# Optimization experiments

Measured on AMD Instinct MI355X. Metric: run time of the kernel, lower is better.

Reference implementation:

```python
import jax, jax.numpy as jnp
import numpy as np

D = 4
R = 6
P = 2 * R + 1          # 13, fine match window
N = P * P              # 169
MR = 12
MP = 2 * MR + 1        # 25, coarse search window
DIL_INT = 15


def corr_sampler(t, r, Pp, dil):
    """SpatialCorrelationSampler(kernel_size=1, patch_size=Pp, dilation_patch=dil).
    t, r: (b,c,h,w). Returns (b,Pp,Pp,h,w): corr[b,p,q,y,x] = sum_c t[b,c,y,x]*r[b,c,y+dil*(p-R),x+dil*(q-R)] (zero pad)."""
    Rr = (Pp - 1) // 2
    pad = Rr * dil
    b, c, h, w = t.shape
    rp = jnp.pad(r, ((0, 0), (0, 0), (pad, pad), (pad, pad)))
    d = (jnp.arange(Pp) - Rr) * dil
    yi = jnp.arange(h)[None, :] + d[:, None] + pad      # (Pp,h)
    xi = jnp.arange(w)[None, :] + d[:, None] + pad      # (Pp,w)
    g = rp[:, :, yi[:, None, :, None], xi[None, :, None, :]]  # (b,c,Pp,Pp,h,w)
    return jnp.einsum('bchw,bcpqhw->bpqhw', t, g)


def bilinear_patch(src, py, px):
    """deform_im2col: bilinear-sample a PxP patch around (x+off_x+dx, y+off_y+dy).
    src (b,c,h,w); py (b,P,1,h,w); px (b,1,P,h,w) float coords. Returns (b,c,P,P,h,w)."""
    b, c, h, w = src.shape
    y0 = jnp.floor(py); x0 = jnp.floor(px)
    wy = py - y0; wx = px - x0
    y0 = y0.astype(jnp.int32); x0 = x0.astype(jnp.int32)

    def corner(yi, xi, wgt):
        valid = (yi >= 0) & (yi < h) & (xi >= 0) & (xi < w)
        yc = jnp.clip(yi, 0, h - 1)
        xc = jnp.clip(xi, 0, w - 1)
        v = jax.vmap(lambda im, a, bb: im[:, a, bb])(src, yc, xc)  # (b,c,P,P,h,w)
        return v * (wgt * valid)[:, None]

    out = corner(y0, x0, (1 - wy) * (1 - wx))
    out = out + corner(y0, x0 + 1, (1 - wy) * wx)
    out = out + corner(y0 + 1, x0, wy * (1 - wx))
    out = out + corner(y0 + 1, x0 + 1, wy * wx)
    return out


def unfold_patches(src, Pp):
    """F.unfold(src, kernel_size=Pp, padding=Rr) -> (b,c,Pp,Pp,h,w)."""
    Rr = (Pp - 1) // 2
    b, c, h, w = src.shape
    sp = jnp.pad(src, ((0, 0), (0, 0), (Rr, Rr), (Rr, Rr)))
    yi = jnp.arange(h)[None, :] + jnp.arange(Pp)[:, None]
    xi = jnp.arange(w)[None, :] + jnp.arange(Pp)[:, None]
    return sp[:, :, yi[:, None, :, None], xi[None, :, None, :]]


def _forward(feats_r, feats_t, quantized_r, nsearch, dirates):
    nref = feats_r.shape[0]
    b, c, h, w = feats_t.shape
    f32 = feats_t.dtype
    dy = (jnp.arange(P) - R).astype(f32)
    gy, gx = jnp.meshgrid(jnp.arange(-MR, MR + 1).astype(f32),
                          jnp.arange(-MR, MR + 1).astype(f32), indexing='ij')
    corrs = []
    py = px = None
    for si in range(nsearch):
        d = dirates[si]
        cc = corr_sampler(feats_t, feats_r[si], MP, d)                     # (b,MP,MP,h,w)
        cc = jax.nn.softmax(cc.reshape(b, MP * MP, h * w), axis=1).reshape(b, MP, MP, h, w)
        off_x = jnp.einsum('bpqhw,pq->bhw', cc, gx) * d                    # soft-argmax offsets
        off_y = jnp.einsum('bpqhw,pq->bhw', cc, gy) * d
        # sample coords: (b,P,1,h,w) / (b,1,P,h,w)
        py = (off_y + jnp.arange(h).astype(f32)[None, :, None])[:, None, None] + dy[:, None, None, None]
        px = (off_x + jnp.arange(w).astype(f32)[None, None, :])[:, None, None] + dy[None, :, None, None]
        col = bilinear_patch(feats_r[si], py, px)                          # (b,c,P,P,h,w)
        corrs.append(jnp.einsum('bchw,bcpqhw->bpqhw', feats_t, col).reshape(b, N, h * w))
    for ind in range(nsearch, nref):
        corrs.append(corr_sampler(feats_t, feats_r[ind], P, 1).reshape(b, N, h * w))
    corr = jax.nn.softmax(jnp.concatenate(corrs, 1), axis=1)               # (b,nref*N,hw)
    qr = quantized_r[:, :, :, ::D, ::D]                                    # prep(): (nref,b,C,h,w)
    cols = []
    for i in range(nsearch):
        # NOTE: faithful to original -- uses offset0 from the LAST coarse-search iteration
        cols.append(bilinear_patch(qr[i], py, px).reshape(b, -1, N, h * w))
    for i in range(nsearch, nref):
        cols.append(unfold_patches(qr[i], P).reshape(b, -1, N, h * w))
    image_uf = jnp.concatenate(cols, 2)                                    # (b,C,nref*N,hw)
    out = jnp.einsum('bnx,bcnx->bcx', corr, image_uf)
    return out.reshape(b, qr.shape[2], h, w)


def reference(feats_r, feats_t, quantized_r, ref_index, current_ind):
    gaps = [int(current_ind) - int(x) for x in np.asarray(ref_index)]
    nsearch = sum(g > DIL_INT for g in gaps)
    dirates = [min(4, g // DIL_INT + 1) for g in gaps if g > DIL_INT]
    return _forward(feats_r, feats_t, quantized_r, nsearch, dirates)


def setup_inputs():
    key = jax.random.key(0)
    k1, k2, k3 = jax.random.split(key, 3)
    feats_r = jax.random.normal(k1, (3, 1, 64, 48, 84), jnp.float32)
    feats_t = jax.random.normal(k2, (1, 64, 48, 84), jnp.float32)
    quantized_r = jax.random.uniform(k3, (3, 1, 32, 192, 336), jnp.float32)
    return dict(feats_r=feats_r, feats_t=feats_t, quantized_r=quantized_r,
                ref_index=np.arange(3), current_ind=16)
```

## Files before the change

### kernel.cpp

```cpp
#include <hip/hip_runtime.h>
#include <math.h>

constexpr int H  = 48;
constexpr int W  = 84;
constexpr int HW = H * W;
constexpr int C  = 64;
constexpr int CQ = 32;
constexpr int QH = 192;
constexpr int QW = 336;
constexpr int NREF = 3;
constexpr int SLG = 176;
constexpr int LGS = 544;
constexpr int S625 = 640;

constexpr int RROWS = NREF * HW;
constexpr int RZERO = RROWS;
constexpr int RLO   = RROWS + 1;
constexpr int TZERO = HW;
constexpr int TLO   = HW + 1;

typedef short bf16x8 __attribute__((ext_vector_type(8)));
typedef float f32x4  __attribute__((ext_vector_type(4)));

#define DEV __device__ __forceinline__

DEV unsigned short f2bf_rn(float f) {
  unsigned int u = __builtin_bit_cast(unsigned int, f);
  u += 0x7FFFu + ((u >> 16) & 1u);
  return (unsigned short)(u >> 16);
}
DEV float bf2f(unsigned short h) {
  unsigned int u = ((unsigned int)h) << 16;
  return __builtin_bit_cast(float, u);
}

DEV float block_sum(float v, float* red) {
  __syncthreads();
#pragma unroll
  for (int o = 32; o > 0; o >>= 1) v += __shfl_down(v, o, 64);
  if ((threadIdx.x & 63) == 0) red[threadIdx.x >> 6] = v;
  __syncthreads();
  return red[0] + red[1] + red[2] + red[3];
}
DEV float block_max(float v, float* red) {
  __syncthreads();
#pragma unroll
  for (int o = 32; o > 0; o >>= 1) v = fmaxf(v, __shfl_down(v, o, 64));
  if ((threadIdx.x & 63) == 0) red[threadIdx.x >> 6] = v;
  __syncthreads();
  return fmaxf(fmaxf(red[0], red[1]), fmaxf(red[2], red[3]));
}

__global__ __launch_bounds__(256) void k_prep(const float* __restrict__ fr,
                                              const float* __restrict__ ft,
                                              const float* __restrict__ q,
                                              float* __restrict__ frT,
                                              float* __restrict__ ftT,
                                              unsigned short* __restrict__ rb,
                                              unsigned short* __restrict__ tb,
                                              unsigned short* __restrict__ qrb) {
  __shared__ float lds[64][65];
  const int mode = blockIdx.y;
  const int tid = threadIdx.x;

  if (mode < 4) {
    const int r = mode;
    const float* src = (r < NREF) ? (fr + (size_t)r * C * HW) : ft;
    float* dstF          = (r < NREF) ? (frT + (size_t)r * HW * C) : ftT;
    unsigned short* dstH = (r < NREF) ? (rb + (size_t)r * HW * C) : tb;
    const size_t loOff   = (size_t)((r < NREF) ? RLO : TLO) * C;
    const int pb = blockIdx.x * 64;
    const int a = tid & 63, b = tid >> 6;
#pragma unroll
    for (int i = 0; i < 16; i++) {
      int c = i * 4 + b;
      lds[c][a] = src[c * HW + pb + a];
    }
    __syncthreads();
#pragma unroll
    for (int i = 0; i < 16; i++) {
      int p = i * 4 + b;
      float v = lds[a][p];
      size_t o = (size_t)(pb + p) * C + a;
      dstF[o] = v;
      unsigned short h = f2bf_rn(v);
      dstH[o] = h;
      dstH[o + loOff] = f2bf_rn(v - bf2f(h));
    }
    if (mode == 3 && blockIdx.x == 0 && tid < 64) {
      rb[(size_t)RZERO * C + tid] = 0;
      rb[(size_t)(RLO + RROWS) * C + tid] = 0;
      tb[(size_t)TZERO * C + tid] = 0;
      tb[(size_t)(TLO + HW) * C + tid] = 0;
    }
  } else {
    const int k = mode - 4;
    const int yq = blockIdx.x;
    if (yq >= H) return;
    unsigned short* qs = (unsigned short*)lds;
    const int c = tid >> 3, xo = tid & 7;
#pragma unroll
    for (int i = 0; i < 11; i++) {
      const int x = xo + 8 * i;
      if (x < W) {
        const float v = q[((size_t)(k * CQ + c) * QH + yq * 4) * QW + x * 4];
        qs[x * CQ + c] = f2bf_rn(v);
      }
    }
    __syncthreads();
    const unsigned int* qsu = (const unsigned int*)qs;
    unsigned int* dst = (unsigned int*)(qrb + (size_t)k * HW * CQ + (size_t)yq * W * CQ);
    for (int o = tid; o < W * CQ / 2; o += 256) dst[o] = qsu[o];
  }
}

__global__ __launch_bounds__(256) void k_mfma(
    const unsigned short* __restrict__ rb, const unsigned short* __restrict__ tb,
    const int* __restrict__ ridx, const int* __restrict__ curp,
    float* __restrict__ lg, float* __restrict__ lg625) {
  const int si = blockIdx.z / 7, pz = blockIdx.z % 7;
  const int gap = curp[0] - ridx[si];
  const bool isSearch = gap > 15;
  const int lane = threadIdx.x & 63, wave = threadIdx.x >> 6;
  const int sub = pz * 4 + wave;
  if (isSearch ? (sub >= 25) : (sub >= 13)) return;

  const int y = blockIdx.y, x0 = blockIdx.x * 16;
  const int fpx = lane & 15, fko = (lane >> 4) * 8;

  const int gapix = (x0 + fpx < W) ? (y * W + x0 + fpx) : TZERO;
  const unsigned short* tbb = tb + (size_t)gapix * C + fko;
  const bf16x8 ah0 = *reinterpret_cast<const bf16x8*>(tbb);
  const bf16x8 ah1 = *reinterpret_cast<const bf16x8*>(tbb + 32);
  const bf16x8 al0 = *reinterpret_cast<const bf16x8*>(tbb + (size_t)TLO * C);
  const bf16x8 al1 = *reinterpret_cast<const bf16x8*>(tbb + (size_t)TLO * C + 32);

  int d = 1, Zoff = 16, NZT = 3, Minv = 65536, qoff = 6, qmax = 13;
  if (isSearch) {
    d = gap / 15 + 1; if (d > 4) d = 4;
    Zoff = (d == 1) ? 16 : (d == 2) ? 32 : 48;
    NZT  = (d == 1) ? 3  : (d == 2) ? 5  : 7;
    Minv = (d == 1) ? 65536 : (d == 2) ? 32768 : (d == 3) ? 21846 : 16384;
    qoff = 12 * d; qmax = 25;
  }
  const int row2 = isSearch ? (y + d * (sub - 12)) : (y + sub - 6);
  const bool rv = (row2 >= 0) && (row2 < H);
  const int rowoff = si * HW + row2 * W;

  float* sb[4];
#pragma unroll
  for (int r = 0; r < 4; r++) {
    const int xl = (lane >> 4) * 4 + r;
    sb[r] = isSearch
        ? (lg625 + ((size_t)si * HW + y * W + x0 + xl) * S625 + sub * 25)
        : (lg + (size_t)(y * W + x0 + xl) * LGS + si * SLG + sub * 13);
  }

  auto gofs = [&](int zt) -> size_t {
    const int z = x0 - Zoff + zt * 16 + fpx;
    const bool v = rv && (z >= 0) && (z < W);
    const int gp = v ? (rowoff + z) : RZERO;
    return (size_t)gp * C + fko;
  };

  size_t o = gofs(0);
  bf16x8 nh0 = *reinterpret_cast<const bf16x8*>(rb + o);
  bf16x8 nh1 = *reinterpret_cast<const bf16x8*>(rb + o + 32);
  bf16x8 nl0 = *reinterpret_cast<const bf16x8*>(rb + o + (size_t)RLO * C);
  bf16x8 nl1 = *reinterpret_cast<const bf16x8*>(rb + o + (size_t)RLO * C + 32);

  for (int zt = 0; zt < NZT; ++zt) {
    const bf16x8 bh0 = nh0, bh1 = nh1, bl0 = nl0, bl1 = nl1;
    if (zt + 1 < NZT) {
      o = gofs(zt + 1);
      nh0 = *reinterpret_cast<const bf16x8*>(rb + o);
      nh1 = *reinterpret_cast<const bf16x8*>(rb + o + 32);
      nl0 = *reinterpret_cast<const bf16x8*>(rb + o + (size_t)RLO * C);
      nl1 = *reinterpret_cast<const bf16x8*>(rb + o + (size_t)RLO * C + 32);
    }
    f32x4 acc = {0.f, 0.f, 0.f, 0.f};
    acc = __builtin_amdgcn_mfma_f32_16x16x32_bf16(ah0, bh0, acc, 0, 0, 0);
    acc = __builtin_amdgcn_mfma_f32_16x16x32_bf16(ah1, bh1, acc, 0, 0, 0);
    acc = __builtin_amdgcn_mfma_f32_16x16x32_bf16(ah0, bl0, acc, 0, 0, 0);
    acc = __builtin_amdgcn_mfma_f32_16x16x32_bf16(ah1, bl1, acc, 0, 0, 0);
    acc = __builtin_amdgcn_mfma_f32_16x16x32_bf16(al0, bh0, acc, 0, 0, 0);
    acc = __builtin_amdgcn_mfma_f32_16x16x32_bf16(al1, bh1, acc, 0, 0, 0);

    const int zbase = x0 - Zoff + zt * 16 + fpx - x0 + qoff;
#pragma unroll
    for (int r = 0; r < 4; r++) {
      const int xl = (lane >> 4) * 4 + r;
      const int qnum = zbase - xl;
      if (qnum >= 0) {
        const int qq = (qnum * Minv) >> 16;
        if (qq * d == qnum && qq < qmax && (x0 + xl) < W) sb[r][qq] = acc[r];
      }
    }
  }
}

__global__ __launch_bounds__(256) void k_pix(
    const float* __restrict__ frT, const float* __restrict__ ftT,
    const unsigned short* __restrict__ qrb, const float* __restrict__ lg,
    const float* __restrict__ lg625,
    const int* __restrict__ ridx, const int* __restrict__ curp,
    float* __restrict__ out) {
  const int pix = blockIdx.x;
  const int y = pix / W, x = pix - y * W;
  const int tid = threadIdx.x;
  const int lane = tid & 63, wave = tid >> 6;

  __shared__ __align__(16) float tl[64];
  __shared__ float C14[14][16];
  __shared__ float sP[4];
  __shared__ float sLs[4];
  __shared__ __align__(16) float lgs[3 * SLG];
  __shared__ __align__(16) float ls6[S625];
  __shared__ float red[4];
  __shared__ int   wloc[640];
  __shared__ float wval[640];
  __shared__ float part[4][32];

  const int cur = curp[0];
  bool srch[NREF];
  int dd[NREF];
  int ls = -1;
#pragma unroll
  for (int k = 0; k < NREF; k++) {
    const int g = cur - ridx[k];
    srch[k] = (g > 15);
    int d = g / 15 + 1;
    dd[k] = d > 4 ? 4 : d;
    if (srch[k]) ls = k;
  }

  if (tid < 64) tl[tid] = ftT[(size_t)pix * C + tid];
  if (tid < 21) lgs[(tid / 7) * SLG + 169 + (tid % 7)] = -1e30f;

  for (int si = 0; si < NREF; ++si) {
    if (!srch[si]) continue;
    const float* Lp = lg625 + ((size_t)si * HW + pix) * S625;
    __syncthreads();
    if (tid < 156)
      *reinterpret_cast<float4*>(&ls6[tid * 4]) =
          *reinterpret_cast<const float4*>(Lp + tid * 4);
    else if (tid == 156) ls6[624] = Lp[624];
    else if (tid < 172) ls6[624 + tid - 156] = -1e30f;

    float m = -1e30f;
    for (int i = tid; i < S625; i += 256) m = fmaxf(m, ls6[i]);
    m = block_max(m, red);
    float se = 0.f, sy = 0.f, sx = 0.f;
    for (int i = tid; i < S625; i += 256) {
      const float e = __expf(ls6[i] - m);
      const int p = (i * 5243) >> 17;
      const int q = i - p * 25;
      se += e; sy += e * (float)(p - 12); sx += e * (float)(q - 12);
    }
    se = block_sum(se, red);
    sy = block_sum(sy, red);
    sx = block_sum(sx, red);
    if (tid == 0) {
      const float inv = 1.f / se;
      const float oy = (float)dd[si] * sy * inv, ox = (float)dd[si] * sx * inv;
      const float fy = (float)y + oy, fx = (float)x + ox;
      const float Y0 = floorf(fy), X0 = floorf(fx);
      sP[0] = Y0; sP[1] = X0; sP[2] = fy - Y0; sP[3] = fx - X0;
      if (si == ls) { sLs[0] = Y0; sLs[1] = X0; sLs[2] = fy - Y0; sLs[3] = fx - X0; }
    }
    __syncthreads();
    const int iY = (int)sP[0], iX = (int)sP[1];
    const float wy = sP[2], wx = sP[3];
    const float* frB = frT + (size_t)si * HW * C;

    if (tid < 224) {
      const int j = tid >> 4, cg = tid & 15;
      const int col = iX - 6 + j;
      const bool cv = (col >= 0) && (col < W);
      const float4 tv = *reinterpret_cast<const float4*>(&tl[cg * 4]);
      float s[14];
#pragma unroll
      for (int i = 0; i < 14; ++i) {
        const int row = iY - 6 + i;
        s[i] = 0.f;
        if (cv && row >= 0 && row < H) {
          const float4 rv4 = *reinterpret_cast<const float4*>(
              frB + (size_t)(row * W + col) * C + cg * 4);
          s[i] = tv.x * rv4.x + tv.y * rv4.y + tv.z * rv4.z + tv.w * rv4.w;
        }
      }
#pragma unroll
      for (int i = 0; i < 14; ++i) {
        s[i] += __shfl_xor(s[i], 1, 64);
        s[i] += __shfl_xor(s[i], 2, 64);
        s[i] += __shfl_xor(s[i], 4, 64);
        s[i] += __shfl_xor(s[i], 8, 64);
      }
      if (cg == 0) {
#pragma unroll
        for (int i = 0; i < 14; ++i) C14[i][j] = s[i];
      }
    }
    __syncthreads();
    for (int it = tid; it < 169; it += 256) {
      const int i = it / 13, j = it - i * 13;
      lgs[si * SLG + it] =
          (1.f - wy) * ((1.f - wx) * C14[i][j] + wx * C14[i][j + 1]) +
          wy * ((1.f - wx) * C14[i + 1][j] + wx * C14[i + 1][j + 1]);
    }
  }

  for (int k = 0; k < NREF; k++) {
    if (srch[k]) continue;
    const float* src = lg + (size_t)pix * LGS + k * SLG;
    for (int it = tid; it < 42; it += 256)
      *reinterpret_cast<float4*>(&lgs[k * SLG + it * 4]) =
          *reinterpret_cast<const float4*>(src + it * 4);
    if (tid == 42) lgs[k * SLG + 168] = src[168];
  }
  __syncthreads();

  float m = -1e30f;
  for (int i = tid; i < 3 * SLG; i += 256) m = fmaxf(m, lgs[i]);
  m = block_max(m, red);
  float se = 0.f;
  for (int i = tid; i < 3 * SLG; i += 256) {
    const float e = __expf(lgs[i] - m);
    lgs[i] = e;
    se += e;
  }
  se = block_sum(se, red);
  const float inv = 1.f / se;

  int bases[NREF], tot = 0;
#pragma unroll
  for (int k = 0; k < NREF; k++) { bases[k] = tot; tot += srch[k] ? 196 : 169; }
  const int NT = (tot + 63) >> 6;

  int liY = 0, liX = 0; float lwy = 0.f, lwx = 0.f;
  if (ls >= 0) { liY = (int)sLs[0]; liX = (int)sLs[1]; lwy = sLs[2]; lwx = sLs[3]; }

  for (int k = 0; k < NREF; k++) {
    const int base = bases[k];
    if (srch[k]) {
      const float* wk = &lgs[k * SLG];
      for (int it = tid; it < 196; it += 256) {
        const int i = it / 14, j = it - i * 14;
        const float a00 = (i < 13 && j < 13) ? wk[i * 13 + j] : 0.f;
        const float a01 = (i < 13 && j >= 1) ? wk[i * 13 + j - 1] : 0.f;
        const float a10 = (i >= 1 && j < 13) ? wk[(i - 1) * 13 + j] : 0.f;
        const float a11 = (i >= 1 && j >= 1) ? wk[(i - 1) * 13 + j - 1] : 0.f;
        const float wv = (1.f - lwy) * ((1.f - lwx) * a00 + lwx * a01) +
                         lwy * ((1.f - lwx) * a10 + lwx * a11);
        const int row = liY + i - 6, col = liX + j - 6;
        const bool v = (unsigned)row < (unsigned)H && (unsigned)col < (unsigned)W;
        wloc[base + it] = v ? (k * HW + row * W + col) : 0;
        wval[base + it] = v ? wv : 0.f;
      }
    } else {
      for (int it = tid; it < 169; it += 256) {
        const int p = it / 13, q = it - p * 13;
        const int row = y + p - 6, col = x + q - 6;
        const bool v = (unsigned)row < (unsigned)H && (unsigned)col < (unsigned)W;
        wloc[base + it] = v ? (k * HW + row * W + col) : 0;
        wval[base + it] = v ? lgs[k * SLG + it] : 0.f;
      }
    }
  }
  for (int e = tot + tid; e < NT * 64; e += 256) { wloc[e] = 0; wval[e] = 0.f; }
  __syncthreads();

  const int c4 = lane & 3, l16 = lane >> 2;
  float a[8] = {0.f, 0.f, 0.f, 0.f, 0.f, 0.f, 0.f, 0.f};
  for (int t = 0; t < NT; ++t) {
    const int e = t * 64 + wave * 16 + l16;
    const float wv = wval[e];
    const int loc = wloc[e];
    const bf16x8 qv = *reinterpret_cast<const bf16x8*>(
        qrb + (size_t)loc * CQ + c4 * 8);
#pragma unroll
    for (int j = 0; j < 8; j++)
      a[j] = fmaf(wv, bf2f((unsigned short)qv[j]), a[j]);
  }
#pragma unroll
  for (int o = 4; o < 64; o <<= 1) {
#pragma unroll
    for (int j = 0; j < 8; j++) a[j] += __shfl_xor(a[j], o, 64);
  }
  if (l16 == 0) {
#pragma unroll
    for (int j = 0; j < 8; j++) part[wave][c4 * 8 + j] = a[j];
  }
  __syncthreads();
  if (tid < 32) {
    const float s = part[0][tid] + part[1][tid] + part[2][tid] + part[3][tid];
    out[(size_t)tid * HW + pix] = s * inv;
  }
}

extern "C" void kernel_launch(void* const* d_in, const int* in_sizes, int n_in,
                              void* d_out, int out_size, void* d_ws, size_t ws_size,
                              hipStream_t stream) {
  (void)in_sizes; (void)n_in; (void)out_size; (void)ws_size;
  const float* fr = (const float*)d_in[0];
  const float* ft = (const float*)d_in[1];
  const float* q  = (const float*)d_in[2];
  const int* ridx = (const int*)d_in[3];
  const int* cur  = (const int*)d_in[4];
  float* out = (float*)d_out;

  char* ws = (char*)d_ws;
  float* frT  = (float*)ws;                  ws += (size_t)NREF * HW * C * 4;
  float* ftT  = (float*)ws;                  ws += (size_t)HW * C * 4;
  unsigned short* rb = (unsigned short*)ws;  ws += (size_t)2 * (NREF * HW + 1) * C * 2;
  unsigned short* tb = (unsigned short*)ws;  ws += (size_t)2 * (HW + 1) * C * 2;
  unsigned short* qrb = (unsigned short*)ws; ws += (size_t)NREF * HW * CQ * 2;
  float* lg    = (float*)ws;                 ws += (size_t)HW * LGS * 4;
  float* lg625 = (float*)ws;                 ws += (size_t)NREF * HW * S625 * 4;

  k_prep<<<dim3(HW / 64, 7), dim3(256), 0, stream>>>(fr, ft, q, frT, ftT,
                                                     rb, tb, qrb);
  k_mfma<<<dim3(6, H, NREF * 7), dim3(256), 0, stream>>>(rb, tb, ridx, cur,
                                                         lg, lg625);
  k_pix<<<dim3(HW), dim3(256), 0, stream>>>(frT, ftT, qrb, lg, lg625,
                                            ridx, cur, out);
}
```

Baseline: 80.96 us.

## Split coarse-search softmax into per-wave kernel and template MFMA search bodies

Adds a k_off kernel that computes each pixel's coarse-search softmax and offset with one wave per pixel using shuffle reductions, and writes the results to a small buffer. k_pix now reads those precomputed offsets, which removes its block-wide reductions and shared staging for the 625 logits. It also prefetches the unsearched logits into registers early. The k_mfma search path is specialised by dilation through templates, giving compile-time loop bounds and shift-based index checks. The cost is one extra kernel launch and a round trip of the offsets through global memory.

```diff
diff --git a/kernel.cpp b/kernel.cpp
--- a/kernel.cpp
+++ b/kernel.cpp
@@ -114,6 +114,131 @@
   }
 }
 
+DEV f32x4 six_mfma(bf16x8 ah0, bf16x8 ah1, bf16x8 al0, bf16x8 al1,
+                   bf16x8 bh0, bf16x8 bh1, bf16x8 bl0, bf16x8 bl1) {
+  f32x4 acc = {0.f, 0.f, 0.f, 0.f};
+  acc = __builtin_amdgcn_mfma_f32_16x16x32_bf16(ah0, bh0, acc, 0, 0, 0);
+  acc = __builtin_amdgcn_mfma_f32_16x16x32_bf16(ah1, bh1, acc, 0, 0, 0);
+  acc = __builtin_amdgcn_mfma_f32_16x16x32_bf16(ah0, bl0, acc, 0, 0, 0);
+  acc = __builtin_amdgcn_mfma_f32_16x16x32_bf16(ah1, bl1, acc, 0, 0, 0);
+  acc = __builtin_amdgcn_mfma_f32_16x16x32_bf16(al0, bh0, acc, 0, 0, 0);
+  acc = __builtin_amdgcn_mfma_f32_16x16x32_bf16(al1, bh1, acc, 0, 0, 0);
+  return acc;
+}
+
+template <int D>
+DEV void sbody(const unsigned short* __restrict__ rb,
+               bf16x8 ah0, bf16x8 ah1, bf16x8 al0, bf16x8 al1,
+               int y, int x0, int sub, int si, int fpx, int lq,
+               float* __restrict__ lg625) {
+  constexpr int Zoff = (D == 1) ? 16 : (D == 2) ? 32 : 48;
+  constexpr int NZT  = (D == 1) ? 3  : (D == 2) ? 5  : 7;
+  const int fko = lq * 8;
+  const int row2 = y + D * (sub - 12);
+  const bool rv = (row2 >= 0) && (row2 < H);
+  const int rowoff = si * HW + row2 * W;
+
+  float* sb[4];
+#pragma unroll
+  for (int r = 0; r < 4; r++) {
+    const int xl = lq * 4 + r;
+    sb[r] = lg625 + ((size_t)si * HW + y * W + x0 + xl) * S625 + sub * 25;
+  }
+
+  auto gofs = [&](int zt) -> size_t {
+    const int z = x0 - Zoff + zt * 16 + fpx;
+    const bool v = rv && (z >= 0) && (z < W);
+    const int gp = v ? (rowoff + z) : RZERO;
+    return (size_t)gp * C + fko;
+  };
+
+  size_t o = gofs(0);
+  bf16x8 nh0 = *reinterpret_cast<const bf16x8*>(rb + o);
+  bf16x8 nh1 = *reinterpret_cast<const bf16x8*>(rb + o + 32);
+  bf16x8 nl0 = *reinterpret_cast<const bf16x8*>(rb + o + (size_t)RLO * C);
+  bf16x8 nl1 = *reinterpret_cast<const bf16x8*>(rb + o + (size_t)RLO * C + 32);
+
+  for (int zt = 0; zt < NZT; ++zt) {
+    const bf16x8 bh0 = nh0, bh1 = nh1, bl0 = nl0, bl1 = nl1;
+    if (zt + 1 < NZT) {
+      o = gofs(zt + 1);
+      nh0 = *reinterpret_cast<const bf16x8*>(rb + o);
+      nh1 = *reinterpret_cast<const bf16x8*>(rb + o + 32);
+      nl0 = *reinterpret_cast<const bf16x8*>(rb + o + (size_t)RLO * C);
+      nl1 = *reinterpret_cast<const bf16x8*>(rb + o + (size_t)RLO * C + 32);
+    }
+    f32x4 acc = six_mfma(ah0, ah1, al0, al1, bh0, bh1, bl0, bl1);
+
+    const int zb = -Zoff + zt * 16 + fpx + 12 * D;
+#pragma unroll
+    for (int r = 0; r < 4; r++) {
+      const int xl = lq * 4 + r;
+      const int qnum = zb - xl;
+      bool ok;
+      int qq;
+      if constexpr (D == 3) {
+        qq = (qnum * 21846) >> 16;
+        ok = (qnum >= 0) && (qq * 3 == qnum) && (qq < 25);
+      } else {
+        constexpr int SH = (D == 4) ? 2 : (D == 2) ? 1 : 0;
+        qq = qnum >> SH;
+        ok = (qnum >= 0) && ((qnum & (D - 1)) == 0) && (qq < 25);
+      }
+      if (ok && (x0 + xl) < W) sb[r][qq] = acc[r];
+    }
+  }
+}
+
+DEV void ubody(const unsigned short* __restrict__ rb,
+               bf16x8 ah0, bf16x8 ah1, bf16x8 al0, bf16x8 al1,
+               int y, int x0, int sub, int si, int fpx, int lq,
+               float* __restrict__ lg) {
+  const int fko = lq * 8;
+  const int row2 = y + sub - 6;
+  const bool rv = (row2 >= 0) && (row2 < H);
+  const int rowoff = si * HW + row2 * W;
+
+  float* sb[4];
+#pragma unroll
+  for (int r = 0; r < 4; r++) {
+    const int xl = lq * 4 + r;
+    sb[r] = lg + (size_t)(y * W + x0 + xl) * LGS + si * SLG + sub * 13;
+  }
+
+  auto gofs = [&](int zt) -> size_t {
+    const int z = x0 - 16 + zt * 16 + fpx;
+    const bool v = rv && (z >= 0) && (z < W);
+    const int gp = v ? (rowoff + z) : RZERO;
+    return (size_t)gp * C + fko;
+  };
+
+  size_t o = gofs(0);
+  bf16x8 nh0 = *reinterpret_cast<const bf16x8*>(rb + o);
+  bf16x8 nh1 = *reinterpret_cast<const bf16x8*>(rb + o + 32);
+  bf16x8 nl0 = *reinterpret_cast<const bf16x8*>(rb + o + (size_t)RLO * C);
+  bf16x8 nl1 = *reinterpret_cast<const bf16x8*>(rb + o + (size_t)RLO * C + 32);
+
+  for (int zt = 0; zt < 3; ++zt) {
+    const bf16x8 bh0 = nh0, bh1 = nh1, bl0 = nl0, bl1 = nl1;
+    if (zt + 1 < 3) {
+      o = gofs(zt + 1);
+      nh0 = *reinterpret_cast<const bf16x8*>(rb + o);
+      nh1 = *reinterpret_cast<const bf16x8*>(rb + o + 32);
+      nl0 = *reinterpret_cast<const bf16x8*>(rb + o + (size_t)RLO * C);
+      nl1 = *reinterpret_cast<const bf16x8*>(rb + o + (size_t)RLO * C + 32);
+    }
+    f32x4 acc = six_mfma(ah0, ah1, al0, al1, bh0, bh1, bl0, bl1);
+
+    const int zb = -16 + zt * 16 + fpx + 6;
+#pragma unroll
+    for (int r = 0; r < 4; r++) {
+      const int xl = lq * 4 + r;
+      const int qq = zb - xl;
+      if (qq >= 0 && qq < 13 && (x0 + xl) < W) sb[r][qq] = acc[r];
+    }
+  }
+}
+
 __global__ __launch_bounds__(256) void k_mfma(
     const unsigned short* __restrict__ rb, const unsigned short* __restrict__ tb,
     const int* __restrict__ ridx, const int* __restrict__ curp,
@@ -126,83 +251,87 @@
   if (isSearch ? (sub >= 25) : (sub >= 13)) return;
 
   const int y = blockIdx.y, x0 = blockIdx.x * 16;
-  const int fpx = lane & 15, fko = (lane >> 4) * 8;
+  const int fpx = lane & 15, lq = lane >> 4;
 
   const int gapix = (x0 + fpx < W) ? (y * W + x0 + fpx) : TZERO;
-  const unsigned short* tbb = tb + (size_t)gapix * C + fko;
+  const unsigned short* tbb = tb + (size_t)gapix * C + lq * 8;
   const bf16x8 ah0 = *reinterpret_cast<const bf16x8*>(tbb);
   const bf16x8 ah1 = *reinterpret_cast<const bf16x8*>(tbb + 32);
   const bf16x8 al0 = *reinterpret_cast<const bf16x8*>(tbb + (size_t)TLO * C);
   const bf16x8 al1 = *reinterpret_cast<const bf16x8*>(tbb + (size_t)TLO * C + 32);
 
-  int d = 1, Zoff = 16, NZT = 3, Minv = 65536, qoff = 6, qmax = 13;
   if (isSearch) {
-    d = gap / 15 + 1; if (d > 4) d = 4;
-    Zoff = (d == 1) ? 16 : (d == 2) ? 32 : 48;
-    NZT  = (d == 1) ? 3  : (d == 2) ? 5  : 7;
-    Minv = (d == 1) ? 65536 : (d == 2) ? 32768 : (d == 3) ? 21846 : 16384;
-    qoff = 12 * d; qmax = 25;
-  }
-  const int row2 = isSearch ? (y + d * (sub - 12)) : (y + sub - 6);
-  const bool rv = (row2 >= 0) && (row2 < H);
-  const int rowoff = si * HW + row2 * W;
-
-  float* sb[4];
-#pragma unroll
-  for (int r = 0; r < 4; r++) {
-    const int xl = (lane >> 4) * 4 + r;
-    sb[r] = isSearch
-        ? (lg625 + ((size_t)si * HW + y * W + x0 + xl) * S625 + sub * 25)
-        : (lg + (size_t)(y * W + x0 + xl) * LGS + si * SLG + sub * 13);
-  }
-
-  auto gofs = [&](int zt) -> size_t {
-    const int z = x0 - Zoff + zt * 16 + fpx;
-    const bool v = rv && (z >= 0) && (z < W);
-    const int gp = v ? (rowoff + z) : RZERO;
-    return (size_t)gp * C + fko;
-  };
-
-  size_t o = gofs(0);
-  bf16x8 nh0 = *reinterpret_cast<const bf16x8*>(rb + o);
-  bf16x8 nh1 = *reinterpret_cast<const bf16x8*>(rb + o + 32);
-  bf16x8 nl0 = *reinterpret_cast<const bf16x8*>(rb + o + (size_t)RLO * C);
-  bf16x8 nl1 = *reinterpret_cast<const bf16x8*>(rb + o + (size_t)RLO * C + 32);
-
-  for (int zt = 0; zt < NZT; ++zt) {
-    const bf16x8 bh0 = nh0, bh1 = nh1, bl0 = nl0, bl1 = nl1;
-    if (zt + 1 < NZT) {
-      o = gofs(zt + 1);
-      nh0 = *reinterpret_cast<const bf16x8*>(rb + o);
-      nh1 = *reinterpret_cast<const bf16x8*>(rb + o + 32);
-      nl0 = *reinterpret_cast<const bf16x8*>(rb + o + (size_t)RLO * C);
-      nl1 = *reinterpret_cast<const bf16x8*>(rb + o + (size_t)RLO * C + 32);
-    }
-    f32x4 acc = {0.f, 0.f, 0.f, 0.f};
-    acc = __builtin_amdgcn_mfma_f32_16x16x32_bf16(ah0, bh0, acc, 0, 0, 0);
-    acc = __builtin_amdgcn_mfma_f32_16x16x32_bf16(ah1, bh1, acc, 0, 0, 0);
-    acc = __builtin_amdgcn_mfma_f32_16x16x32_bf16(ah0, bl0, acc, 0, 0, 0);
-    acc = __builtin_amdgcn_mfma_f32_16x16x32_bf16(ah1, bl1, acc, 0, 0, 0);
-    acc = __builtin_amdgcn_mfma_f32_16x16x32_bf16(al0, bh0, acc, 0, 0, 0);
-    acc = __builtin_amdgcn_mfma_f32_16x16x32_bf16(al1, bh1, acc, 0, 0, 0);
-
-    const int zbase = x0 - Zoff + zt * 16 + fpx - x0 + qoff;
-#pragma unroll
-    for (int r = 0; r < 4; r++) {
-      const int xl = (lane >> 4) * 4 + r;
-      const int qnum = zbase - xl;
-      if (qnum >= 0) {
-        const int qq = (qnum * Minv) >> 16;
-        if (qq * d == qnum && qq < qmax && (x0 + xl) < W) sb[r][qq] = acc[r];
-      }
-    }
+    int d = gap / 15 + 1; if (d > 4) d = 4;
+    switch (d) {
+      case 1: sbody<1>(rb, ah0, ah1, al0, al1, y, x0, sub, si, fpx, lq, lg625); break;
+      case 2: sbody<2>(rb, ah0, ah1, al0, al1, y, x0, sub, si, fpx, lq, lg625); break;
+      case 3: sbody<3>(rb, ah0, ah1, al0, al1, y, x0, sub, si, fpx, lq, lg625); break;
+      default: sbody<4>(rb, ah0, ah1, al0, al1, y, x0, sub, si, fpx, lq, lg625); break;
+    }
+  } else {
+    ubody(rb, ah0, ah1, al0, al1, y, x0, sub, si, fpx, lq, lg);
+  }
+}
+
+__global__ __launch_bounds__(256) void k_off(
+    const float* __restrict__ lg625,
+    const int* __restrict__ ridx, const int* __restrict__ curp,
+    float* __restrict__ samp) {
+  const int si = blockIdx.y;
+  const int gap = curp[0] - ridx[si];
+  if (gap <= 15) return;
+  int d = gap / 15 + 1; if (d > 4) d = 4;
+
+  const int lane = threadIdx.x & 63, wave = threadIdx.x >> 6;
+  const int pix = blockIdx.x * 4 + wave;
+  const float* Lp = lg625 + ((size_t)si * HW + pix) * S625;
+
+  float v[10];
+#pragma unroll
+  for (int k = 0; k < 10; k++) {
+    const int idx = k * 64 + lane;
+    v[k] = (idx < 625) ? Lp[idx] : -1e30f;
+  }
+  float m = v[0];
+#pragma unroll
+  for (int k = 1; k < 10; k++) m = fmaxf(m, v[k]);
+#pragma unroll
+  for (int o = 1; o < 64; o <<= 1) m = fmaxf(m, __shfl_xor(m, o, 64));
+
+  float se = 0.f, sy = 0.f, sx = 0.f;
+#pragma unroll
+  for (int k = 0; k < 10; k++) {
+    const int idx = k * 64 + lane;
+    if (idx < 625) {
+      const float e = __expf(v[k] - m);
+      const int p = (idx * 5243) >> 17;
+      const int q = idx - p * 25;
+      se += e;
+      sy += e * (float)(p - 12);
+      sx += e * (float)(q - 12);
+    }
+  }
+#pragma unroll
+  for (int o = 1; o < 64; o <<= 1) {
+    se += __shfl_xor(se, o, 64);
+    sy += __shfl_xor(sy, o, 64);
+    sx += __shfl_xor(sx, o, 64);
+  }
+  if (lane == 0) {
+    const float inv = 1.f / se;
+    const float oy = (float)d * sy * inv, ox = (float)d * sx * inv;
+    const int y = pix / W, x = pix - y * W;
+    const float fy = (float)y + oy, fx = (float)x + ox;
+    const float Y0 = floorf(fy), X0 = floorf(fx);
+    *reinterpret_cast<float4*>(samp + ((size_t)si * HW + pix) * 4) =
+        make_float4(Y0, X0, fy - Y0, fx - X0);
   }
 }
 
 __global__ __launch_bounds__(256) void k_pix(
     const float* __restrict__ frT, const float* __restrict__ ftT,
     const unsigned short* __restrict__ qrb, const float* __restrict__ lg,
-    const float* __restrict__ lg625,
+    const float* __restrict__ samp,
     const int* __restrict__ ridx, const int* __restrict__ curp,
     float* __restrict__ out) {
   const int pix = blockIdx.x;
@@ -212,10 +341,7 @@
 
   __shared__ __align__(16) float tl[64];
   __shared__ float C14[14][16];
-  __shared__ float sP[4];
-  __shared__ float sLs[4];
   __shared__ __align__(16) float lgs[3 * SLG];
-  __shared__ __align__(16) float ls6[S625];
   __shared__ float red[4];
   __shared__ int   wloc[640];
   __shared__ float wval[640];
@@ -223,54 +349,36 @@
 
   const int cur = curp[0];
   bool srch[NREF];
-  int dd[NREF];
   int ls = -1;
 #pragma unroll
   for (int k = 0; k < NREF; k++) {
-    const int g = cur - ridx[k];
-    srch[k] = (g > 15);
-    int d = g / 15 + 1;
-    dd[k] = d > 4 ? 4 : d;
+    srch[k] = (cur - ridx[k]) > 15;
     if (srch[k]) ls = k;
   }
 
   if (tid < 64) tl[tid] = ftT[(size_t)pix * C + tid];
   if (tid < 21) lgs[(tid / 7) * SLG + 169 + (tid % 7)] = -1e30f;
-
+  float4 upre[NREF];
+  float ulast[NREF];
+#pragma unroll
+  for (int k = 0; k < NREF; k++) {
+    upre[k] = make_float4(0.f, 0.f, 0.f, 0.f); ulast[k] = 0.f;
+    if (!srch[k]) {
+      const float* src = lg + (size_t)pix * LGS + k * SLG;
+      if (tid < 42) upre[k] = *reinterpret_cast<const float4*>(src + tid * 4);
+      else if (tid == 42) ulast[k] = src[168];
+    }
+  }
+  __syncthreads();
+
+  int liY = 0, liX = 0;
+  float lwy = 0.f, lwx = 0.f;
   for (int si = 0; si < NREF; ++si) {
     if (!srch[si]) continue;
-    const float* Lp = lg625 + ((size_t)si * HW + pix) * S625;
-    __syncthreads();
-    if (tid < 156)
-      *reinterpret_cast<float4*>(&ls6[tid * 4]) =
-          *reinterpret_cast<const float4*>(Lp + tid * 4);
-    else if (tid == 156) ls6[624] = Lp[624];
-    else if (tid < 172) ls6[624 + tid - 156] = -1e30f;
-
-    float m = -1e30f;
-    for (int i = tid; i < S625; i += 256) m = fmaxf(m, ls6[i]);
-    m = block_max(m, red);
-    float se = 0.f, sy = 0.f, sx = 0.f;
-    for (int i = tid; i < S625; i += 256) {
-      const float e = __expf(ls6[i] - m);
-      const int p = (i * 5243) >> 17;
-      const int q = i - p * 25;
-      se += e; sy += e * (float)(p - 12); sx += e * (float)(q - 12);
-    }
-    se = block_sum(se, red);
-    sy = block_sum(sy, red);
-    sx = block_sum(sx, red);
-    if (tid == 0) {
-      const float inv = 1.f / se;
-      const float oy = (float)dd[si] * sy * inv, ox = (float)dd[si] * sx * inv;
-      const float fy = (float)y + oy, fx = (float)x + ox;
-      const float Y0 = floorf(fy), X0 = floorf(fx);
-      sP[0] = Y0; sP[1] = X0; sP[2] = fy - Y0; sP[3] = fx - X0;
-      if (si == ls) { sLs[0] = Y0; sLs[1] = X0; sLs[2] = fy - Y0; sLs[3] = fx - X0; }
-    }
-    __syncthreads();
-    const int iY = (int)sP[0], iX = (int)sP[1];
-    const float wy = sP[2], wx = sP[3];
+    const float4 sp = *reinterpret_cast<const float4*>(samp + ((size_t)si * HW + pix) * 4);
+    const int iY = (int)sp.x, iX = (int)sp.y;
+    const float wy = sp.z, wx = sp.w;
+    if (si == ls) { liY = iY; liX = iX; lwy = wy; lwx = wx; }
     const float* frB = frT + (size_t)si * HW * C;
 
     if (tid < 224) {
@@ -308,17 +416,16 @@
           (1.f - wy) * ((1.f - wx) * C14[i][j] + wx * C14[i][j + 1]) +
           wy * ((1.f - wx) * C14[i + 1][j] + wx * C14[i + 1][j + 1]);
     }
-  }
-
+    __syncthreads();
+  }
+
+#pragma unroll
   for (int k = 0; k < NREF; k++) {
-    if (srch[k]) continue;
-    const float* src = lg + (size_t)pix * LGS + k * SLG;
-    for (int it = tid; it < 42; it += 256)
-      *reinterpret_cast<float4*>(&lgs[k * SLG + it * 4]) =
-          *reinterpret_cast<const float4*>(src + it * 4);
-    if (tid == 42) lgs[k * SLG + 168] = src[168];
-  }
-  __syncthreads();
+    if (!srch[k]) {
+      if (tid < 42) *reinterpret_cast<float4*>(&lgs[k * SLG + tid * 4]) = upre[k];
+      else if (tid == 42) lgs[k * SLG + 168] = ulast[k];
+    }
+  }
 
   float m = -1e30f;
   for (int i = tid; i < 3 * SLG; i += 256) m = fmaxf(m, lgs[i]);
@@ -336,9 +443,6 @@
 #pragma unroll
   for (int k = 0; k < NREF; k++) { bases[k] = tot; tot += srch[k] ? 196 : 169; }
   const int NT = (tot + 63) >> 6;
-
-  int liY = 0, liX = 0; float lwy = 0.f, lwx = 0.f;
-  if (ls >= 0) { liY = (int)sLs[0]; liX = (int)sLs[1]; lwy = sLs[2]; lwx = sLs[3]; }
 
   for (int k = 0; k < NREF; k++) {
     const int base = bases[k];
@@ -417,11 +521,13 @@
   unsigned short* qrb = (unsigned short*)ws; ws += (size_t)NREF * HW * CQ * 2;
   float* lg    = (float*)ws;                 ws += (size_t)HW * LGS * 4;
   float* lg625 = (float*)ws;                 ws += (size_t)NREF * HW * S625 * 4;
+  float* samp  = (float*)ws;                 ws += (size_t)NREF * HW * 4 * 4;
 
   k_prep<<<dim3(HW / 64, 7), dim3(256), 0, stream>>>(fr, ft, q, frT, ftT,
                                                      rb, tb, qrb);
   k_mfma<<<dim3(6, H, NREF * 7), dim3(256), 0, stream>>>(rb, tb, ridx, cur,
                                                          lg, lg625);
-  k_pix<<<dim3(HW), dim3(256), 0, stream>>>(frT, ftT, qrb, lg, lg625,
+  k_off<<<dim3(HW / 4, NREF), dim3(256), 0, stream>>>(lg625, ridx, cur, samp);
+  k_pix<<<dim3(HW), dim3(256), 0, stream>>>(frT, ftT, qrb, lg, samp,
                                             ridx, cur, out);
 }
```

New measurement: 121.6 us. +50.2%, slower.
